# Optimization experiments

Measured on AMD Instinct MI355X. Metric: run time of the kernel, lower is better.

## Reference

```python
import jax, jax.numpy as jnp
import numpy as np

B, T, C = 2, 2048, 1024
N_HEAD = 16
HEAD_DIM = C // N_HEAD

def setup_inputs() -> dict:
    key = jax.random.key(0)
    k1, k2, k3 = jax.random.split(key, 3)
    x = jax.random.normal(k1, (B, T, C), dtype=jnp.float32)
    # Dense kernel init scale ~ 1/sqrt(fan_in) for stable softmax
    w_attn = jax.random.normal(k2, (C, 3 * C), dtype=jnp.float32) / np.sqrt(C)
    w_proj = jax.random.normal(k3, (C, C), dtype=jnp.float32) / np.sqrt(C)
    return {"x": x, "w_attn": w_attn, "w_proj": w_proj}

def reference(x, w_attn, w_proj):
    Bc, Tc, Cc = x.shape
    # QKV projection (use_bias=False)
    qkv = x @ w_attn  # [B, T, 3C]
    q, k, v = jnp.split(qkv, 3, axis=-1)
    # [B, T, C] -> [B, H, T, D]
    def heads(a):
        return a.reshape(Bc, Tc, N_HEAD, HEAD_DIM).swapaxes(1, 2)
    q, k, v = heads(q), heads(k), heads(v)
    scale = 1.0 / jnp.sqrt(jnp.asarray(HEAD_DIM, dtype=x.dtype))
    attn = jnp.einsum('bhqd,bhkd->bhqk', q, k) * scale  # [B, H, T, T]
    attn = jax.nn.softmax(attn, axis=-1)
    # dropout=0.0 / deterministic -> identity
    y = jnp.einsum('bhqk,bhkd->bhqd', attn, v)  # [B, H, T, D]
    y = y.swapaxes(1, 2).reshape(Bc, Tc, Cc)
    return y @ w_proj  # output projection, no bias, dropout identity
```

## Files before the change

### kernel.cpp

```cpp
#include <hip/hip_runtime.h>
#include <hip/hip_bf16.h>

#define B_   2
#define T_   2048
#define C_   1024
#define NH_  16
#define HD_  64

typedef __attribute__((ext_vector_type(8))) short short8;
typedef __attribute__((ext_vector_type(4))) float float4_;
typedef __attribute__((ext_vector_type(4))) _Float16 half4_;
typedef __attribute__((ext_vector_type(2))) __fp16  fp16x2;
typedef __attribute__((ext_vector_type(4))) unsigned short ushort4_;

static __device__ __forceinline__ unsigned short f2bf(float f) {
    union { float f; unsigned u; } v; v.f = f;
    unsigned r = v.u + 0x7fffu + ((v.u >> 16) & 1u);
    return (unsigned short)(r >> 16);
}

static __device__ __forceinline__ void g2l16(const void* g, void* l) {
    __builtin_amdgcn_global_load_lds(
        (const __attribute__((address_space(1))) void*)g,
        (__attribute__((address_space(3))) void*)l, 16, 0, 0);
}

__global__ __launch_bounds__(256) void prep(
    const float* __restrict__ x,      unsigned short* __restrict__ xb,
    const float* __restrict__ wA,     unsigned short* __restrict__ wTa,
    const float* __restrict__ wP,     unsigned short* __restrict__ wTp)
{
    const int t = threadIdx.x;
    int blk = blockIdx.x;
    if (blk < 2048) {
        int i = blk * 256 + t;
        const float4* p = (const float4*)x + (size_t)i * 2;
        float4 a = p[0], b = p[1];
        short8 o;
        o[0]=f2bf(a.x); o[1]=f2bf(a.y); o[2]=f2bf(a.z); o[3]=f2bf(a.w);
        o[4]=f2bf(b.x); o[5]=f2bf(b.y); o[6]=f2bf(b.z); o[7]=f2bf(b.w);
        *((short8*)xb + i) = o;
        return;
    }
    blk -= 2048;
    const float* in; unsigned short* out; int Cc;
    if (blk < 16 * 48) { in = wA; out = wTa; Cc = 3072; }
    else               { blk -= 16 * 48; in = wP; out = wTp; Cc = 1024; }
    const int r0 = (blk % 16) * 64, c0 = (blk / 16) * 64;
    const int R = 1024;
    __shared__ __align__(16) unsigned short Ts[64][72];
    #pragma unroll
    for (int cc = 0; cc < 2; ++cc) {
        int c = cc * 256 + t;
        int r = c >> 3, col = (c & 7) * 8;
        const float* p = in + (size_t)(r0 + r) * Cc + c0 + col;
        #pragma unroll
        for (int i = 0; i < 8; ++i) Ts[col + i][r] = f2bf(p[i]);
    }
    __syncthreads();
    #pragma unroll
    for (int cc = 0; cc < 2; ++cc) {
        int c = cc * 256 + t;
        int cr = c >> 3, oc = (c & 7) * 8;
        uint4 v = *(const uint4*)(&Ts[cr][oc]);
        *(uint4*)(out + (size_t)(c0 + cr) * R + r0 + oc) = v;
    }
}

template <bool C_F32, int BM, bool WRITE_VT>
__global__ __launch_bounds__(256) void gemm_bt(
    const unsigned short* __restrict__ A,
    const unsigned short* __restrict__ Bt,
    void* __restrict__ Cv, unsigned short* __restrict__ vt,
    int M, int N, int K)
{
    __shared__ __align__(16) unsigned short As[BM * 32];
    __shared__ __align__(16) unsigned short Bs[128 * 32];
    const int t = threadIdx.x, lane = t & 63, w = t >> 6;
    const int quad = lane >> 4, ln = lane & 15;
    const int bm = blockIdx.x, bn = blockIdx.y;
    constexpr int NI = (BM == 128) ? 4 : 2;
    const int mw = (BM == 128) ? (w & 1) * 64 : 0;
    const int nw = (BM == 128) ? (w >> 1) * 64 : w * 32;
    float4_ acc[4][NI] = {};

    constexpr int AROWS = BM / 4;
    const unsigned short* Ag = A  + (size_t)(bm * BM + w * AROWS + (lane >> 2)) * K + (lane & 3) * 8;
    const unsigned short* Bg = Bt + (size_t)(bn * 128 + w * 32 + (lane >> 2)) * K + (lane & 3) * 8;
    unsigned short* lA = &As[(w * AROWS) * 32 + lane * 8];
    unsigned short* lB = &Bs[(w * 32) * 32 + lane * 8];

    for (int k0 = 0; k0 < K; k0 += 32) {
        g2l16(Ag + k0, lA);
        if (BM == 128) g2l16(Ag + (size_t)16 * K + k0, lA + 16 * 32);
        g2l16(Bg + k0,                  lB);
        g2l16(Bg + (size_t)16 * K + k0, lB + 16 * 32);
        __syncthreads();
        short8 a[4], b[NI];
        #pragma unroll
        for (int i = 0; i < 4; ++i)
            a[i] = *(const short8*)(&As[(mw + i * 16 + ln) * 32 + quad * 8]);
        #pragma unroll
        for (int i = 0; i < NI; ++i)
            b[i] = *(const short8*)(&Bs[(nw + i * 16 + ln) * 32 + quad * 8]);
        #pragma unroll
        for (int mi = 0; mi < 4; ++mi)
            #pragma unroll
            for (int ni = 0; ni < NI; ++ni)
                acc[mi][ni] = __builtin_amdgcn_mfma_f32_16x16x32_bf16(
                    a[mi], b[ni], acc[mi][ni], 0, 0, 0);
        __syncthreads();
    }

    const int row0 = bm * BM + mw + quad * 4;
    const int col0 = bn * 128 + nw + ln;
    #pragma unroll
    for (int mi = 0; mi < 4; ++mi)
        #pragma unroll
        for (int ni = 0; ni < NI; ++ni) {
            #pragma unroll
            for (int i = 0; i < 4; ++i) {
                size_t idx = (size_t)(row0 + mi * 16 + i) * N + col0 + ni * 16;
                if (C_F32) ((float*)Cv)[idx] = acc[mi][ni][i];
                else       ((unsigned short*)Cv)[idx] = f2bf(acc[mi][ni][i]);
            }
            if (WRITE_VT && col0 + ni * 16 >= 2 * C_) {
                int d     = col0 + ni * 16 - 2 * C_;
                int token = row0 + mi * 16;
                int b     = token >> 11, tloc = token & 2047;
                union { fp16x2 h2[2]; ushort4_ u4; } pk;
                pk.h2[0] = __builtin_amdgcn_cvt_pkrtz(acc[mi][ni][0], acc[mi][ni][1]);
                pk.h2[1] = __builtin_amdgcn_cvt_pkrtz(acc[mi][ni][2], acc[mi][ni][3]);
                *(ushort4_*)(vt + ((size_t)b * 1024 + d) * T_ + tloc) = pk.u4;
            }
        }
}

__global__ __launch_bounds__(256) void attn(
    const unsigned short* __restrict__ qkv,
    const unsigned short* __restrict__ vt,
    unsigned short* __restrict__ Y)
{
    __shared__ __align__(16) unsigned short Qs[128][72];
    __shared__ __align__(16) unsigned short Ks[64][72];
    __shared__ __align__(16) unsigned short Vs[64][72];

    const int t = threadIdx.x;
    const int qt = blockIdx.x, bh = blockIdx.y;
    const int b = bh >> 4, h = bh & 15;
    const int lane = t & 63, w = t >> 6;
    const int quad = lane >> 4, ln = lane & 15;

    const unsigned short* Qg  = qkv + (size_t)b * T_ * (3 * C_) + (size_t)h * HD_;
    const unsigned short* Kg  = Qg + C_;
    const unsigned short* Vtg = vt + (size_t)bh * HD_ * T_;

    #pragma unroll
    for (int cc = 0; cc < 4; ++cc) {
        int c = cc * 256 + t;
        int r = c >> 3, col = (c & 7) * 8;
        *(uint4*)(&Qs[r][col]) = *(const uint4*)(Qg + (size_t)(qt * 128 + r) * (3 * C_) + col);
    }

    const int r0 = t >> 3, c0v = (t & 7) * 8;
    const int r1 = r0 + 32;

    uint4 kr0 = *(const uint4*)(Kg + (size_t)r0 * (3 * C_) + c0v);
    uint4 kr1 = *(const uint4*)(Kg + (size_t)r1 * (3 * C_) + c0v);
    uint4 vr0 = *(const uint4*)(Vtg + (size_t)r0 * T_ + c0v);
    uint4 vr1 = *(const uint4*)(Vtg + (size_t)r1 * T_ + c0v);

    __syncthreads();

    short8 qf[2][2];
    #pragma unroll
    for (int qm = 0; qm < 2; ++qm)
        #pragma unroll
        for (int dh = 0; dh < 2; ++dh)
            qf[qm][dh] = *(const short8*)(&Qs[w * 32 + qm * 16 + ln][dh * 32 + quad * 8]);

    float4_ ot[4][2] = {};
    float ls[2] = {0.f, 0.f};
    const float C1 = 0.125f * 1.44269504f;
    const float C2 = 8.0f * 1.44269504f;

    for (int kt = 0; kt < T_ / 64; ++kt) {
        if (kt) __syncthreads();
        *(uint4*)(&Ks[r0][c0v]) = kr0;
        *(uint4*)(&Ks[r1][c0v]) = kr1;
        *(uint4*)(&Vs[r0][c0v]) = vr0;
        *(uint4*)(&Vs[r1][c0v]) = vr1;
        __syncthreads();

        if (kt + 1 < T_ / 64) {
            int kb = (kt + 1) * 64;
            kr0 = *(const uint4*)(Kg + (size_t)(kb + r0) * (3 * C_) + c0v);
            kr1 = *(const uint4*)(Kg + (size_t)(kb + r1) * (3 * C_) + c0v);
            vr0 = *(const uint4*)(Vtg + (size_t)r0 * T_ + kb + c0v);
            vr1 = *(const uint4*)(Vtg + (size_t)r1 * T_ + kb + c0v);
        }

        half4_ pf[4][2];
        #pragma unroll
        for (int ct = 0; ct < 4; ++ct) {
            short8 kb0 = *(const short8*)(&Ks[ct * 16 + ln][quad * 8]);
            short8 kb1 = *(const short8*)(&Ks[ct * 16 + ln][32 + quad * 8]);
            #pragma unroll
            for (int qm = 0; qm < 2; ++qm) {
                float4_ st = {};
                st = __builtin_amdgcn_mfma_f32_16x16x32_bf16(kb0, qf[qm][0], st, 0, 0, 0);
                st = __builtin_amdgcn_mfma_f32_16x16x32_bf16(kb1, qf[qm][1], st, 0, 0, 0);
                float p0 = __builtin_amdgcn_exp2f(st[0] * C1 - C2);
                float p1 = __builtin_amdgcn_exp2f(st[1] * C1 - C2);
                float p2 = __builtin_amdgcn_exp2f(st[2] * C1 - C2);
                float p3 = __builtin_amdgcn_exp2f(st[3] * C1 - C2);
                ls[qm] += (p0 + p1) + (p2 + p3);
                union { fp16x2 h2[2]; half4_ h4; } u;
                u.h2[0] = __builtin_amdgcn_cvt_pkrtz(p0, p1);
                u.h2[1] = __builtin_amdgcn_cvt_pkrtz(p2, p3);
                pf[ct][qm] = u.h4;
            }
        }

        #pragma unroll
        for (int dt = 0; dt < 4; ++dt)
            #pragma unroll
            for (int ct = 0; ct < 4; ++ct) {
                half4_ va = *(const half4_*)(&Vs[dt * 16 + ln][ct * 16 + quad * 4]);
                #pragma unroll
                for (int qm = 0; qm < 2; ++qm)
                    ot[dt][qm] = __builtin_amdgcn_mfma_f32_16x16x16f16(
                        va, pf[ct][qm], ot[dt][qm], 0, 0, 0);
            }
    }

    #pragma unroll
    for (int qm = 0; qm < 2; ++qm) {
        ls[qm] += __shfl_xor(ls[qm], 16, 64);
        ls[qm] += __shfl_xor(ls[qm], 32, 64);
    }

    #pragma unroll
    for (int qm = 0; qm < 2; ++qm) {
        unsigned short* Yr = Y + ((size_t)b * T_ + qt * 128 + w * 32 + qm * 16 + ln) * C_ + h * HD_;
        float inv = 1.0f / ls[qm];
        #pragma unroll
        for (int dt = 0; dt < 4; ++dt)
            #pragma unroll
            for (int i = 0; i < 4; ++i)
                Yr[dt * 16 + quad * 4 + i] = f2bf(ot[dt][qm][i] * inv);
    }
}

extern "C" void kernel_launch(void* const* d_in, const int* in_sizes, int n_in,
                              void* d_out, int out_size, void* d_ws, size_t ws_size,
                              hipStream_t stream)
{
    const float* x      = (const float*)d_in[0];
    const float* w_attn = (const float*)d_in[1];
    const float* w_proj = (const float*)d_in[2];
    float* out = (float*)d_out;

    unsigned short* qkv = (unsigned short*)d_ws;
    unsigned short* y   = qkv + (size_t)4096 * 3072;
    unsigned short* wTa = y   + (size_t)4096 * 1024;
    unsigned short* wTp = wTa + (size_t)3072 * 1024;
    unsigned short* vt  = wTp + (size_t)1024 * 1024;
    unsigned short* xb  = y;

    prep<<<2048 + 16 * 48 + 16 * 16, 256, 0, stream>>>(x, xb, w_attn, wTa, w_proj, wTp);

    gemm_bt<false, 128, true><<<dim3(32, 24), 256, 0, stream>>>(
        xb, wTa, qkv, vt, 4096, 3072, 1024);
    attn<<<dim3(16, 32), 256, 0, stream>>>(qkv, vt, y);
    gemm_bt<true, 64, false><<<dim3(64, 8), 256, 0, stream>>>(
        y, wTp, out, nullptr, 4096, 1024, 1024);
}
```

Measured before the change: 197.0 us.

## Split attention over key halves with a merge kernel and skip V row stores

The attention kernel now splits the key sequence into two halves along a new grid dimension. Each half writes unnormalized fp16 partial outputs and row sums, and a new merge kernel adds them and normalizes. This doubles the number of attention blocks (512 to 1024) to fill more CUs, at the cost of an extra kernel launch and extra partial-output traffic. The QKV GEMM also stops writing the V columns to the row-major qkv buffer, since only the transposed copy is consumed.

```diff
diff --git a/kernel.cpp b/kernel.cpp
--- a/kernel.cpp
+++ b/kernel.cpp
@@ -118,13 +118,8 @@
     for (int mi = 0; mi < 4; ++mi)
         #pragma unroll
         for (int ni = 0; ni < NI; ++ni) {
-            #pragma unroll
-            for (int i = 0; i < 4; ++i) {
-                size_t idx = (size_t)(row0 + mi * 16 + i) * N + col0 + ni * 16;
-                if (C_F32) ((float*)Cv)[idx] = acc[mi][ni][i];
-                else       ((unsigned short*)Cv)[idx] = f2bf(acc[mi][ni][i]);
-            }
-            if (WRITE_VT && col0 + ni * 16 >= 2 * C_) {
+            bool isv = WRITE_VT && (col0 + ni * 16 >= 2 * C_);
+            if (isv) {
                 int d     = col0 + ni * 16 - 2 * C_;
                 int token = row0 + mi * 16;
                 int b     = token >> 11, tloc = token & 2047;
@@ -132,6 +127,13 @@
                 pk.h2[0] = __builtin_amdgcn_cvt_pkrtz(acc[mi][ni][0], acc[mi][ni][1]);
                 pk.h2[1] = __builtin_amdgcn_cvt_pkrtz(acc[mi][ni][2], acc[mi][ni][3]);
                 *(ushort4_*)(vt + ((size_t)b * 1024 + d) * T_ + tloc) = pk.u4;
+            } else {
+                #pragma unroll
+                for (int i = 0; i < 4; ++i) {
+                    size_t idx = (size_t)(row0 + mi * 16 + i) * N + col0 + ni * 16;
+                    if (C_F32) ((float*)Cv)[idx] = acc[mi][ni][i];
+                    else       ((unsigned short*)Cv)[idx] = f2bf(acc[mi][ni][i]);
+                }
             }
         }
 }
@@ -139,21 +141,22 @@
 __global__ __launch_bounds__(256) void attn(
     const unsigned short* __restrict__ qkv,
     const unsigned short* __restrict__ vt,
-    unsigned short* __restrict__ Y)
+    unsigned short* __restrict__ op,
+    float* __restrict__ lp)
 {
     __shared__ __align__(16) unsigned short Qs[128][72];
     __shared__ __align__(16) unsigned short Ks[64][72];
     __shared__ __align__(16) unsigned short Vs[64][72];
 
     const int t = threadIdx.x;
-    const int qt = blockIdx.x, bh = blockIdx.y;
+    const int qt = blockIdx.x, bh = blockIdx.y, s = blockIdx.z;
     const int b = bh >> 4, h = bh & 15;
     const int lane = t & 63, w = t >> 6;
     const int quad = lane >> 4, ln = lane & 15;
 
     const unsigned short* Qg  = qkv + (size_t)b * T_ * (3 * C_) + (size_t)h * HD_;
-    const unsigned short* Kg  = Qg + C_;
-    const unsigned short* Vtg = vt + (size_t)bh * HD_ * T_;
+    const unsigned short* Kg  = Qg + C_ + (size_t)(s * (T_ / 2)) * (3 * C_);
+    const unsigned short* Vtg = vt + (size_t)bh * HD_ * T_ + s * (T_ / 2);
 
     #pragma unroll
     for (int cc = 0; cc < 4; ++cc) {
@@ -184,7 +187,7 @@
     const float C1 = 0.125f * 1.44269504f;
     const float C2 = 8.0f * 1.44269504f;
 
-    for (int kt = 0; kt < T_ / 64; ++kt) {
+    for (int kt = 0; kt < T_ / 128; ++kt) {
         if (kt) __syncthreads();
         *(uint4*)(&Ks[r0][c0v]) = kr0;
         *(uint4*)(&Ks[r1][c0v]) = kr1;
@@ -192,7 +195,7 @@
         *(uint4*)(&Vs[r1][c0v]) = vr1;
         __syncthreads();
 
-        if (kt + 1 < T_ / 64) {
+        if (kt + 1 < T_ / 128) {
             int kb = (kt + 1) * 64;
             kr0 = *(const uint4*)(Kg + (size_t)(kb + r0) * (3 * C_) + c0v);
             kr1 = *(const uint4*)(Kg + (size_t)(kb + r1) * (3 * C_) + c0v);
@@ -242,14 +245,48 @@
 
     #pragma unroll
     for (int qm = 0; qm < 2; ++qm) {
-        unsigned short* Yr = Y + ((size_t)b * T_ + qt * 128 + w * 32 + qm * 16 + ln) * C_ + h * HD_;
-        float inv = 1.0f / ls[qm];
-        #pragma unroll
-        for (int dt = 0; dt < 4; ++dt)
-            #pragma unroll
-            for (int i = 0; i < 4; ++i)
-                Yr[dt * 16 + quad * 4 + i] = f2bf(ot[dt][qm][i] * inv);
-    }
+        int q = qt * 128 + w * 32 + qm * 16 + ln;
+        unsigned short* Or = op + (size_t)s * (4096 * 1024)
+                           + ((size_t)b * T_ + q) * C_ + h * HD_;
+        #pragma unroll
+        for (int dt = 0; dt < 4; ++dt) {
+            union { fp16x2 h2[2]; ushort4_ u4; } pk;
+            pk.h2[0] = __builtin_amdgcn_cvt_pkrtz(ot[dt][qm][0], ot[dt][qm][1]);
+            pk.h2[1] = __builtin_amdgcn_cvt_pkrtz(ot[dt][qm][2], ot[dt][qm][3]);
+            *(ushort4_*)(Or + dt * 16 + quad * 4) = pk.u4;
+        }
+        if (quad == 0)
+            lp[((size_t)s * (B_ * NH_) + bh) * T_ + q] = ls[qm];
+    }
+}
+
+__global__ __launch_bounds__(256) void merge(
+    const unsigned short* __restrict__ op,
+    const float* __restrict__ lp,
+    unsigned short* __restrict__ y)
+{
+    const size_t i = ((size_t)blockIdx.x * 256 + threadIdx.x) * 8;
+    const int row = (int)(i >> 10);
+    const int c   = (int)(i & 1023);
+    const int b = row >> 11, q = row & 2047, h = c >> 6;
+    const int bh = b * 16 + h;
+    float l = lp[(size_t)bh * T_ + q] + lp[((size_t)B_ * NH_ + bh) * T_ + q];
+    float inv = 1.0f / l;
+    ushort4_ a0 = *(const ushort4_*)(op + i);
+    ushort4_ a1 = *(const ushort4_*)(op + (size_t)4096 * 1024 + i);
+    ushort4_ b0 = *(const ushort4_*)(op + i + 4);
+    ushort4_ b1 = *(const ushort4_*)(op + (size_t)4096 * 1024 + i + 4);
+    unsigned short o[8];
+    #pragma unroll
+    for (int j = 0; j < 4; ++j) {
+        union { unsigned short u; __fp16 hh; } x0, x1, y0, y1;
+        x0.u = a0[j]; x1.u = a1[j];
+        y0.u = b0[j]; y1.u = b1[j];
+        o[j]     = f2bf(((float)x0.hh + (float)x1.hh) * inv);
+        o[j + 4] = f2bf(((float)y0.hh + (float)y1.hh) * inv);
+    }
+    *(ushort4_*)(y + i)     = *(ushort4_*)&o[0];
+    *(ushort4_*)(y + i + 4) = *(ushort4_*)&o[4];
 }
 
 extern "C" void kernel_launch(void* const* d_in, const int* in_sizes, int n_in,
@@ -266,13 +303,17 @@
     unsigned short* wTa = y   + (size_t)4096 * 1024;
     unsigned short* wTp = wTa + (size_t)3072 * 1024;
     unsigned short* vt  = wTp + (size_t)1024 * 1024;
+    unsigned short* op  = vt  + (size_t)B_ * NH_ * HD_ * T_;
+    float* lp           = (float*)(op + (size_t)2 * 4096 * 1024);
     unsigned short* xb  = y;
 
     prep<<<2048 + 16 * 48 + 16 * 16, 256, 0, stream>>>(x, xb, w_attn, wTa, w_proj, wTp);
 
     gemm_bt<false, 128, true><<<dim3(32, 24), 256, 0, stream>>>(
         xb, wTa, qkv, vt, 4096, 3072, 1024);
-    attn<<<dim3(16, 32), 256, 0, stream>>>(qkv, vt, y);
+    attn<<<dim3(16, 32, 2), 256, 0, stream>>>(qkv, vt, op, lp);
+    merge<<<4096 * 1024 / 8 / 256, 256, 0, stream>>>(op, lp, y);
+
     gemm_bt<true, 64, false><<<dim3(64, 8), 256, 0, stream>>>(
         y, wTp, out, nullptr, 4096, 1024, 1024);
 }
```

Result: slower. 205.2 us (+4.2%).
